# Optimization experiments

Hardware: AMD Instinct MI355X
Metric: run time of the kernel (lower is better)

## Reference

```python
import jax, jax.numpy as jnp
import numpy as np

NUM_CLASSES = 80
STRIDES = (8, 16, 32)
IMG_H, IMG_W = 480, 640
TOPK = 10


def _make_anchors():
    anchors, strides_t = [], []
    for s in STRIDES:
        fH, fW = IMG_H // s, IMG_W // s
        gy, gx = jnp.meshgrid(jnp.arange(fH, dtype=jnp.float32), jnp.arange(fW, dtype=jnp.float32), indexing='ij')
        grid = jnp.stack([gx, gy], axis=-1).reshape(-1, 2)
        anchors.append((grid + 0.5) * s)
        strides_t.append(jnp.full((fH * fW,), float(s), dtype=jnp.float32))
    return jnp.concatenate(anchors, 0), jnp.concatenate(strides_t, 0)


def _bce_logits(x, t):
    # stable BCEWithLogits, matches torch: max(x,0) - x*t + log(1+exp(-|x|))
    return jnp.maximum(x, 0.0) - x * t + jnp.log1p(jnp.exp(-jnp.abs(x)))


def _iou_loss(pred, gt, eps=1e-7):
    pcx, pcy, pw, ph = pred[..., 0], pred[..., 1], pred[..., 2], pred[..., 3]
    gcx, gcy, gw, gh = gt[..., 0], gt[..., 1], gt[..., 2], gt[..., 3]
    px1, py1, px2, py2 = pcx - pw / 2, pcy - ph / 2, pcx + pw / 2, pcy + ph / 2
    gx1, gy1, gx2, gy2 = gcx - gw / 2, gcy - gh / 2, gcx + gw / 2, gcy + gh / 2
    iw = jnp.maximum(jnp.minimum(px2, gx2) - jnp.maximum(px1, gx1), 0.0)
    ih = jnp.maximum(jnp.minimum(py2, gy2) - jnp.maximum(py1, gy1), 0.0)
    inter = iw * ih
    union = (px2 - px1) * (py2 - py1) + (gx2 - gx1) * (gy2 - gy1) - inter
    iou = inter / (union + eps)
    cx_d = (pcx - gcx) ** 2 + (pcy - gcy) ** 2
    diag = (jnp.maximum(px2, gx2) - jnp.minimum(px1, gx1)) ** 2 + (jnp.maximum(py2, gy2) - jnp.minimum(py1, gy1)) ** 2 + eps
    v = (4.0 / jnp.pi ** 2) * (jnp.arctan(gw / (gh + eps)) - jnp.arctan(pw / (ph + eps))) ** 2
    alpha = v / (1.0 - iou + v + eps)
    return 1.0 - iou + cx_d / diag + alpha * v


def _yolox_loss(out0, out1, out2, targets):
    anchors, strides_t = _make_anchors()          # [A,2], [A]
    all_out = jnp.concatenate([out0, out1, out2], axis=1)  # [B,A,5+C]
    B, A, _ = all_out.shape
    T = targets.shape[0]
    s = strides_t[None, :, None]                  # [1,A,1]
    pred_xy = (jax.nn.sigmoid(all_out[..., :2]) + anchors[None] / s) * s
    pred_wh = jnp.exp(jnp.minimum(all_out[..., 2:4], 4.0)) * s
    pred_boxes = jnp.concatenate([pred_xy, pred_wh], axis=-1)  # [B,A,4]

    t_img = targets[:, 0].astype(jnp.int32)       # [T]
    gt_cls = targets[:, 1].astype(jnp.int32)      # [T]
    scale = jnp.array([IMG_W, IMG_H, IMG_W, IMG_H], dtype=jnp.float32)
    gt_boxes = targets[:, 2:6] * scale            # [T,4] in pixels

    # per-GT top-k closest anchors (center distance)
    dist = jnp.sqrt((anchors[None, :, 0] - gt_boxes[:, 0:1]) ** 2 + (anchors[None, :, 1] - gt_boxes[:, 1:2]) ** 2)  # [T,A]
    _, topk_idx = jax.lax.top_k(-dist, TOPK)      # [T,TOPK]

    flat_idx = (t_img[:, None] * A + topk_idx).reshape(-1)
    t_ids = jnp.broadcast_to(jnp.arange(T, dtype=jnp.int32)[:, None], (T, TOPK)).reshape(-1)
    matched_t = jnp.full((B * A,), -1, dtype=jnp.int32).at[flat_idx].max(t_ids).reshape(B, A)
    fg = matched_t >= 0                           # [B,A]
    fg_f = fg.astype(jnp.float32)
    matched_box = jnp.where(fg[..., None], gt_boxes[jnp.maximum(matched_t, 0)], 0.0)  # [B,A,4]

    n_fg_b = fg_f.sum(axis=1)                     # [B]
    n_fg_total = n_fg_b.sum()
    denom_b = jnp.maximum(n_fg_b, 1.0)

    # obj loss: per-image mean then /B == global mean over [B,A]
    loss_obj = _bce_logits(all_out[..., 4], fg_f).mean()

    # box loss: per-image mean over fg anchors, summed over images
    box_l = _iou_loss(pred_boxes, matched_box)    # [B,A]
    loss_box = ((box_l * fg_f).sum(axis=1) / denom_b).sum()

    # cls loss: original uses the FIRST GT's class for all fg anchors of the image
    first_t = jnp.full((B,), T, dtype=jnp.int32).at[t_img].min(jnp.arange(T, dtype=jnp.int32))
    cls_first = gt_cls[jnp.minimum(first_t, T - 1)]            # [B]
    cls_t = jax.nn.one_hot(cls_first, NUM_CLASSES, dtype=jnp.float32)  # [B,C]
    bce_c = _bce_logits(all_out[..., 5:], cls_t[:, None, :])   # [B,A,C]
    loss_cls = ((bce_c * fg_f[..., None]).sum(axis=(1, 2)) / (denom_b * NUM_CLASSES)).sum()

    loss_obj = loss_obj  # already /B via global mean
    norm = jnp.maximum(1.0, n_fg_total / B)
    total = loss_obj + loss_cls / norm + 5.0 * loss_box / norm
    return total


def setup_inputs() -> dict:
    key = jax.random.key(0)
    k0, k1, k2, k3, k4, k5, k6 = jax.random.split(key, 7)
    B, T = 64, 1024
    CH = 5 + NUM_CLASSES
    out0 = jax.random.normal(k0, (B, (IMG_H // 8) * (IMG_W // 8), CH), dtype=jnp.float32)
    out1 = jax.random.normal(k1, (B, (IMG_H // 16) * (IMG_W // 16), CH), dtype=jnp.float32)
    out2 = jax.random.normal(k2, (B, (IMG_H // 32) * (IMG_W // 32), CH), dtype=jnp.float32)
    t_img = jax.random.randint(k3, (T,), 0, B).astype(jnp.float32)
    t_cls = jax.random.randint(k4, (T,), 0, NUM_CLASSES).astype(jnp.float32)
    cxcy = jax.random.uniform(k5, (T, 2), minval=0.1, maxval=0.9, dtype=jnp.float32)
    wh = jax.random.uniform(k6, (T, 2), minval=0.05, maxval=0.3, dtype=jnp.float32)
    targets = jnp.concatenate([t_img[:, None], t_cls[:, None], cxcy, wh], axis=1)
    return {"out0": out0, "out1": out1, "out2": out2, "targets": targets}


def reference(out0, out1, out2, targets):
    return _yolox_loss(out0, out1, out2, targets)
```

## Files before the change

kernel.cpp:

```cpp
#include <hip/hip_runtime.h>
#include <math.h>

#define NUM_CL 80
#define A0 4800
#define A1 1200
#define A2 300
#define A_TOTAL 6300
#define B_IMG 64
#define T_TGT 1024
#define TOPK 10
#define RT 403200
#define NCHUNK 25
#define CHUNK_A 252
#define NBLK (B_IMG * NCHUNK)

__device__ __forceinline__ void anchor_of(int a, float& ax, float& ay, float& s) {
    if (a < A0) {
        int gx = a % 80, gy = a / 80;
        ax = (gx + 0.5f) * 8.0f; ay = (gy + 0.5f) * 8.0f; s = 8.0f;
    } else if (a < A0 + A1) {
        int al = a - A0;
        int gx = al % 40, gy = al / 40;
        ax = (gx + 0.5f) * 16.0f; ay = (gy + 0.5f) * 16.0f; s = 16.0f;
    } else {
        int al = a - (A0 + A1);
        int gx = al % 20, gy = al / 20;
        ax = (gx + 0.5f) * 32.0f; ay = (gy + 0.5f) * 32.0f; s = 32.0f;
    }
}

__device__ __forceinline__ const float* elem_ptr(const float* o0, const float* o1,
                                                 const float* o2, int b, int a) {
    if (a < A0)      return o0 + ((size_t)b * A0 + a) * 85;
    if (a < A0 + A1) return o1 + ((size_t)b * A1 + (a - A0)) * 85;
    return o2 + ((size_t)b * A2 + (a - A0 - A1)) * 85;
}

__device__ __forceinline__ float bce_fast(float x, float t) {
    return fmaxf(x, 0.0f) - x * t + __logf(1.0f + __expf(-fabsf(x)));
}

__global__ void init_kernel(int* __restrict__ matched, int* __restrict__ first_t) {
    int i = blockIdx.x * blockDim.x + threadIdx.x;
    int4* m4 = (int4*)matched;
    if (i < RT / 4) m4[i] = make_int4(-1, -1, -1, -1);
    if (i < B_IMG) first_t[i] = T_TGT;
}

__global__ void match_kernel(const float* __restrict__ tg,
                             int* __restrict__ matched, int* __restrict__ first_t) {
    int t = blockIdx.x * blockDim.x + threadIdx.x;
    if (t >= T_TGT) return;
    int img = (int)tg[t * 6 + 0];
    float gcx = tg[t * 6 + 2] * 640.0f;
    float gcy = tg[t * 6 + 3] * 480.0f;
    atomicMin(&first_t[img], t);

    float d[TOPK];
    int id[TOPK];
#pragma unroll
    for (int j = 0; j < TOPK; ++j) { d[j] = INFINITY; id[j] = 0x7FFFFFFF; }

    auto scan_scale = [&](float s, int W, int H, int base, int r) {
        int nx = (int)floorf(gcx / s);
        int ny = (int)floorf(gcy / s);
        for (int dy = -r; dy <= r; ++dy) {
            int iy = ny + dy;
            if (iy < 0 || iy >= H) continue;
            float ay = (iy + 0.5f) * s;
            float ddy = ay - gcy;
            for (int dx = -r; dx <= r; ++dx) {
                int ix = nx + dx;
                if (ix < 0 || ix >= W) continue;
                float ax = (ix + 0.5f) * s;
                float ddx = ax - gcx;
                float dist = sqrtf(ddx * ddx + ddy * ddy);
                int ai = base + iy * W + ix;
                if (dist < d[TOPK - 1] || (dist == d[TOPK - 1] && ai < id[TOPK - 1])) {
                    float cd = dist; int ci = ai;
#pragma unroll
                    for (int j = 0; j < TOPK; ++j) {
                        bool sw = (cd < d[j]) || (cd == d[j] && ci < id[j]);
                        float od = d[j]; int oi = id[j];
                        if (sw) { d[j] = cd; id[j] = ci; cd = od; ci = oi; }
                    }
                }
            }
        }
    };
    scan_scale(8.0f,  80, 60, 0, 2);
    scan_scale(16.0f, 40, 30, A0, 1);
    scan_scale(32.0f, 20, 15, A0 + A1, 1);

#pragma unroll
    for (int k = 0; k < TOPK; ++k)
        atomicMax(&matched[img * A_TOTAL + id[k]], t);
}

__global__ __launch_bounds__(256) void main_kernel(
        const float* __restrict__ o0, const float* __restrict__ o1,
        const float* __restrict__ o2, const float* __restrict__ tg,
        const int* __restrict__ matched, const int* __restrict__ first_t,
        float4* __restrict__ partials) {
    int blk = blockIdx.x;
    int b = blk / NCHUNK;
    int chunk = blk - b * NCHUNK;
    int tid = threadIdx.x, lane = tid & 63, wid = tid >> 6;
    int a = chunk * CHUNK_A + tid;

    __shared__ unsigned fglist[CHUNK_A];
    __shared__ int nfg_s;
    __shared__ float wred[4][4];
    if (tid == 0) nfg_s = 0;
    __syncthreads();

    float sp = 0.0f;
    if (tid < CHUNK_A) {
        const float* p = elem_ptr(o0, o1, o2, b, a);
        float x4 = p[4];
        sp = fmaxf(x4, 0.0f) + __logf(1.0f + __expf(-fabsf(x4)));
        int m = matched[b * A_TOTAL + a];
        if (m >= 0) {
            int idx = atomicAdd(&nfg_s, 1);
            fglist[idx] = (unsigned)a | ((unsigned)m << 16);
        }
    }
#pragma unroll
    for (int off = 32; off >= 1; off >>= 1) sp += __shfl_xor(sp, off, 64);
    if (lane == 0) wred[0][wid] = sp;
    __syncthreads();
    int nfg = nfg_s;

    float boxacc = 0.0f, clsacc = 0.0f, objfix = 0.0f;
    if (nfg > 0) {
        int ft = first_t[b];
        if (ft > T_TGT - 1) ft = T_TGT - 1;
        int clsb = (int)tg[ft * 6 + 1];

        for (int i = wid; i < nfg; i += 4) {
            unsigned e = fglist[i];
            int a2 = e & 0xFFFF;
            int m  = (int)(e >> 16);
            const float* p = elem_ptr(o0, o1, o2, b, a2);
            float v0 = p[lane];
            float v1 = (lane < 21) ? p[64 + lane] : 0.0f;

            float cl = 0.0f;
            if (lane >= 5) cl = bce_fast(v0, ((lane - 5) == clsb) ? 1.0f : 0.0f);
            if (lane < 21) cl += bce_fast(v1, ((lane + 59) == clsb) ? 1.0f : 0.0f);
#pragma unroll
            for (int off = 32; off >= 1; off >>= 1) cl += __shfl_xor(cl, off, 64);

            float x0 = __shfl(v0, 0, 64), x1 = __shfl(v0, 1, 64);
            float x2 = __shfl(v0, 2, 64), x3 = __shfl(v0, 3, 64);
            float x4 = __shfl(v0, 4, 64);

            float ax, ay, s;
            anchor_of(a2, ax, ay, s);
            float sig0 = 1.0f / (1.0f + expf(-x0));
            float sig1 = 1.0f / (1.0f + expf(-x1));
            float pcx = (sig0 + ax / s) * s;
            float pcy = (sig1 + ay / s) * s;
            float pw = expf(fminf(x2, 4.0f)) * s;
            float ph = expf(fminf(x3, 4.0f)) * s;

            float gcx = tg[m * 6 + 2] * 640.0f;
            float gcy = tg[m * 6 + 3] * 480.0f;
            float gw  = tg[m * 6 + 4] * 640.0f;
            float gh  = tg[m * 6 + 5] * 480.0f;

            const float eps = 1e-7f;
            float px1 = pcx - pw * 0.5f, py1 = pcy - ph * 0.5f;
            float px2 = pcx + pw * 0.5f, py2 = pcy + ph * 0.5f;
            float gx1 = gcx - gw * 0.5f, gy1 = gcy - gh * 0.5f;
            float gx2 = gcx + gw * 0.5f, gy2 = gcy + gh * 0.5f;
            float iw = fmaxf(fminf(px2, gx2) - fmaxf(px1, gx1), 0.0f);
            float ih = fmaxf(fminf(py2, gy2) - fmaxf(py1, gy1), 0.0f);
            float inter = iw * ih;
            float uni = (px2 - px1) * (py2 - py1) + (gx2 - gx1) * (gy2 - gy1) - inter;
            float iou = inter / (uni + eps);
            float dcx = pcx - gcx, dcy = pcy - gcy;
            float cxd = dcx * dcx + dcy * dcy;
            float dmx = fmaxf(px2, gx2) - fminf(px1, gx1);
            float dmy = fmaxf(py2, gy2) - fminf(py1, gy1);
            float diag = dmx * dmx + dmy * dmy + eps;
            float da = atanf(gw / (gh + eps)) - atanf(pw / (ph + eps));
            float v = 0.40528473456935109f * (da * da);
            float alpha = v / (1.0f - iou + v + eps);
            float box_l = 1.0f - iou + cxd / diag + alpha * v;

            boxacc += box_l;
            clsacc += cl;
            objfix += -x4;
        }
    }
    if (lane == 0) {
        wred[1][wid] = boxacc;
        wred[2][wid] = clsacc;
        wred[3][wid] = objfix;
    }
    __syncthreads();

    if (tid == 0) {
        float4 r;
        r.x = wred[0][0] + wred[0][1] + wred[0][2] + wred[0][3]
            + wred[3][0] + wred[3][1] + wred[3][2] + wred[3][3];
        r.y = wred[1][0] + wred[1][1] + wred[1][2] + wred[1][3];
        r.z = wred[2][0] + wred[2][1] + wred[2][2] + wred[2][3];
        r.w = (float)nfg;
        partials[blk] = r;
    }
}

__global__ void finalize_kernel(const float4* __restrict__ partials,
                                float* __restrict__ out) {
    int b = threadIdx.x;
    float ob = 0.0f, bx = 0.0f, cl = 0.0f, nf = 0.0f;
#pragma unroll
    for (int c = 0; c < NCHUNK; ++c) {
        float4 r = partials[b * NCHUNK + c];
        ob += r.x; bx += r.y; cl += r.z; nf += r.w;
    }
    float denom = fmaxf(nf, 1.0f);
    bx /= denom;
    cl /= (denom * (float)NUM_CL);
    float nt = nf;
#pragma unroll
    for (int off = 32; off >= 1; off >>= 1) {
        bx += __shfl_xor(bx, off, 64);
        cl += __shfl_xor(cl, off, 64);
        ob += __shfl_xor(ob, off, 64);
        nt += __shfl_xor(nt, off, 64);
    }
    if (b == 0) {
        float loss_obj = ob / (float)RT;
        float norm = fmaxf(1.0f, nt / (float)B_IMG);
        out[0] = loss_obj + cl / norm + 5.0f * bx / norm;
    }
}

extern "C" void kernel_launch(void* const* d_in, const int* in_sizes, int n_in,
                              void* d_out, int out_size, void* d_ws, size_t ws_size,
                              hipStream_t stream) {
    const float* o0 = (const float*)d_in[0];
    const float* o1 = (const float*)d_in[1];
    const float* o2 = (const float*)d_in[2];
    const float* tg = (const float*)d_in[3];

    int* matched     = (int*)d_ws;
    int* first_t     = matched + RT;
    float4* partials = (float4*)(first_t + B_IMG);
    float* out = (float*)d_out;

    init_kernel<<<(RT / 4 + 255) / 256, 256, 0, stream>>>(matched, first_t);
    match_kernel<<<T_TGT / 64, 64, 0, stream>>>(tg, matched, first_t);
    main_kernel<<<NBLK, 256, 0, stream>>>(o0, o1, o2, tg, matched, first_t, partials);
    finalize_kernel<<<1, 64, 0, stream>>>(partials, out);
}
```

Before: 201.6 us.

## Fuse target matching into main kernel with per-block shared-memory match table

Removes the init and match kernels and the global matched buffer. Each main-kernel block now scans all targets to find those for its image, recomputes the top-k anchor matching for them, and records only matches inside its own anchor chunk in shared memory. This saves two launches and the global init and atomic traffic. In exchange, the matching work is repeated by all 25 chunk blocks of each image, and each block first reads the whole target array.

```diff
diff --git a/kernel.cpp b/kernel.cpp
--- a/kernel.cpp
+++ b/kernel.cpp
@@ -40,78 +40,84 @@
     return fmaxf(x, 0.0f) - x * t + __logf(1.0f + __expf(-fabsf(x)));
 }
 
-__global__ void init_kernel(int* __restrict__ matched, int* __restrict__ first_t) {
-    int i = blockIdx.x * blockDim.x + threadIdx.x;
-    int4* m4 = (int4*)matched;
-    if (i < RT / 4) m4[i] = make_int4(-1, -1, -1, -1);
-    if (i < B_IMG) first_t[i] = T_TGT;
-}
-
-__global__ void match_kernel(const float* __restrict__ tg,
-                             int* __restrict__ matched, int* __restrict__ first_t) {
-    int t = blockIdx.x * blockDim.x + threadIdx.x;
-    if (t >= T_TGT) return;
-    int img = (int)tg[t * 6 + 0];
-    float gcx = tg[t * 6 + 2] * 640.0f;
-    float gcy = tg[t * 6 + 3] * 480.0f;
-    atomicMin(&first_t[img], t);
-
-    float d[TOPK];
-    int id[TOPK];
-#pragma unroll
-    for (int j = 0; j < TOPK; ++j) { d[j] = INFINITY; id[j] = 0x7FFFFFFF; }
-
-    auto scan_scale = [&](float s, int W, int H, int base, int r) {
-        int nx = (int)floorf(gcx / s);
-        int ny = (int)floorf(gcy / s);
-        for (int dy = -r; dy <= r; ++dy) {
-            int iy = ny + dy;
-            if (iy < 0 || iy >= H) continue;
-            float ay = (iy + 0.5f) * s;
-            float ddy = ay - gcy;
-            for (int dx = -r; dx <= r; ++dx) {
-                int ix = nx + dx;
-                if (ix < 0 || ix >= W) continue;
-                float ax = (ix + 0.5f) * s;
-                float ddx = ax - gcx;
-                float dist = sqrtf(ddx * ddx + ddy * ddy);
-                int ai = base + iy * W + ix;
-                if (dist < d[TOPK - 1] || (dist == d[TOPK - 1] && ai < id[TOPK - 1])) {
-                    float cd = dist; int ci = ai;
-#pragma unroll
-                    for (int j = 0; j < TOPK; ++j) {
-                        bool sw = (cd < d[j]) || (cd == d[j] && ci < id[j]);
-                        float od = d[j]; int oi = id[j];
-                        if (sw) { d[j] = cd; id[j] = ci; cd = od; ci = oi; }
-                    }
-                }
-            }
-        }
-    };
-    scan_scale(8.0f,  80, 60, 0, 2);
-    scan_scale(16.0f, 40, 30, A0, 1);
-    scan_scale(32.0f, 20, 15, A0 + A1, 1);
-
-#pragma unroll
-    for (int k = 0; k < TOPK; ++k)
-        atomicMax(&matched[img * A_TOTAL + id[k]], t);
-}
-
 __global__ __launch_bounds__(256) void main_kernel(
         const float* __restrict__ o0, const float* __restrict__ o1,
         const float* __restrict__ o2, const float* __restrict__ tg,
-        const int* __restrict__ matched, const int* __restrict__ first_t,
         float4* __restrict__ partials) {
     int blk = blockIdx.x;
     int b = blk / NCHUNK;
     int chunk = blk - b * NCHUNK;
     int tid = threadIdx.x, lane = tid & 63, wid = tid >> 6;
-    int a = chunk * CHUNK_A + tid;
-
+    int abase = chunk * CHUNK_A;
+    int a = abase + tid;
+
+    __shared__ int tlist[T_TGT];
+    __shared__ int ntgt_s, first_t_s, nfg_s;
+    __shared__ int matched_s[CHUNK_A];
     __shared__ unsigned fglist[CHUNK_A];
-    __shared__ int nfg_s;
     __shared__ float wred[4][4];
-    if (tid == 0) nfg_s = 0;
+
+    if (tid == 0) { ntgt_s = 0; first_t_s = T_TGT; nfg_s = 0; }
+    if (tid < CHUNK_A) matched_s[tid] = -1;
+    __syncthreads();
+
+    for (int t = tid; t < T_TGT; t += 256) {
+        if ((int)tg[t * 6 + 0] == b) {
+            int i = atomicAdd(&ntgt_s, 1);
+            tlist[i] = t;
+            atomicMin(&first_t_s, t);
+        }
+    }
+    __syncthreads();
+    int ntgt = ntgt_s;
+
+    for (int i = tid; i < ntgt; i += 256) {
+        int t = tlist[i];
+        float gcx = tg[t * 6 + 2] * 640.0f;
+        float gcy = tg[t * 6 + 3] * 480.0f;
+
+        float d[TOPK];
+        int id[TOPK];
+#pragma unroll
+        for (int j = 0; j < TOPK; ++j) { d[j] = INFINITY; id[j] = 0x7FFFFFFF; }
+
+        auto scan_scale = [&](float s, int W, int H, int base, int r) {
+            int nx = (int)floorf(gcx / s);
+            int ny = (int)floorf(gcy / s);
+            for (int dy = -r; dy <= r; ++dy) {
+                int iy = ny + dy;
+                if (iy < 0 || iy >= H) continue;
+                float ay = (iy + 0.5f) * s;
+                float ddy = ay - gcy;
+                for (int dx = -r; dx <= r; ++dx) {
+                    int ix = nx + dx;
+                    if (ix < 0 || ix >= W) continue;
+                    float ax = (ix + 0.5f) * s;
+                    float ddx = ax - gcx;
+                    float dist = sqrtf(ddx * ddx + ddy * ddy);
+                    int ai = base + iy * W + ix;
+                    if (dist < d[TOPK - 1] || (dist == d[TOPK - 1] && ai < id[TOPK - 1])) {
+                        float cd = dist; int ci = ai;
+#pragma unroll
+                        for (int j = 0; j < TOPK; ++j) {
+                            bool sw = (cd < d[j]) || (cd == d[j] && ci < id[j]);
+                            float od = d[j]; int oi = id[j];
+                            if (sw) { d[j] = cd; id[j] = ci; cd = od; ci = oi; }
+                        }
+                    }
+                }
+            }
+        };
+        scan_scale(8.0f,  80, 60, 0, 2);
+        scan_scale(16.0f, 40, 30, A0, 1);
+        scan_scale(32.0f, 20, 15, A0 + A1, 1);
+
+#pragma unroll
+        for (int k = 0; k < TOPK; ++k) {
+            int rel = id[k] - abase;
+            if (rel >= 0 && rel < CHUNK_A) atomicMax(&matched_s[rel], t);
+        }
+    }
     __syncthreads();
 
     float sp = 0.0f;
@@ -119,7 +125,7 @@
         const float* p = elem_ptr(o0, o1, o2, b, a);
         float x4 = p[4];
         sp = fmaxf(x4, 0.0f) + __logf(1.0f + __expf(-fabsf(x4)));
-        int m = matched[b * A_TOTAL + a];
+        int m = matched_s[tid];
         if (m >= 0) {
             int idx = atomicAdd(&nfg_s, 1);
             fglist[idx] = (unsigned)a | ((unsigned)m << 16);
@@ -133,7 +139,7 @@
 
     float boxacc = 0.0f, clsacc = 0.0f, objfix = 0.0f;
     if (nfg > 0) {
-        int ft = first_t[b];
+        int ft = first_t_s;
         if (ft > T_TGT - 1) ft = T_TGT - 1;
         int clsb = (int)tg[ft * 6 + 1];
 
@@ -247,13 +253,9 @@
     const float* o2 = (const float*)d_in[2];
     const float* tg = (const float*)d_in[3];
 
-    int* matched     = (int*)d_ws;
-    int* first_t     = matched + RT;
-    float4* partials = (float4*)(first_t + B_IMG);
+    float4* partials = (float4*)d_ws;
     float* out = (float*)d_out;
 
-    init_kernel<<<(RT / 4 + 255) / 256, 256, 0, stream>>>(matched, first_t);
-    match_kernel<<<T_TGT / 64, 64, 0, stream>>>(tg, matched, first_t);
-    main_kernel<<<NBLK, 256, 0, stream>>>(o0, o1, o2, tg, matched, first_t, partials);
+    main_kernel<<<NBLK, 256, 0, stream>>>(o0, o1, o2, tg, partials);
     finalize_kernel<<<1, 64, 0, stream>>>(partials, out);
 }
```

Result: faster. 196.2 us (-2.7%).
